# Kernel tuning notes

Measured on AMD Instinct MI355X. Metric: run time of the kernel, lower is better.

The kernel has to match this reference:

```python
import jax, jax.numpy as jnp
import numpy as np

N_WIRES = 9
N_QRAM_LAYERS = 3
N_QCLS_LAYERS = 5

X = jnp.array([[0, 1], [1, 0]], dtype=jnp.complex64)
CNOT = jnp.array([[1, 0, 0, 0], [0, 1, 0, 0], [0, 0, 0, 1], [0, 0, 1, 0]], dtype=jnp.complex64)


def _rx(t):
    c = jnp.cos(t / 2)
    s = jnp.sin(t / 2)
    # works for scalar t -> (2,2) or batched t [B] -> (B,2,2)
    return jnp.stack([jnp.stack([c + 0j, -1j * s], -1), jnp.stack([-1j * s, c + 0j], -1)], -2)


def _ry(t):
    c = jnp.cos(t / 2)
    s = jnp.sin(t / 2)
    return jnp.stack([jnp.stack([c, -s], -1), jnp.stack([s, c], -1)], -2).astype(jnp.complex64)


def _rz(t):
    e = jnp.exp(-0.5j * t)
    f = jnp.exp(0.5j * t)
    z = jnp.zeros_like(e)
    return jnp.stack([jnp.stack([e, z], -1), jnp.stack([z, f], -1)], -2)


def _rot(phi, theta, omega):
    # PennyLane Rot(phi, theta, omega) = RZ(omega) @ RY(theta) @ RZ(phi)
    return _rz(omega) @ _ry(theta) @ _rz(phi)


def _crz(t):
    e = jnp.exp(-0.5j * t)
    f = jnp.exp(0.5j * t)
    one = jnp.ones((), e.dtype)
    return jnp.diag(jnp.stack([one, one, e, f]))


def _crx(t):
    return jnp.eye(4, dtype=jnp.complex64).at[2:, 2:].set(_rx(t))


def apply_1q(state, U, w):
    # state: [B] + (2,)*N_WIRES ; wire w -> axis 1+w
    s = jnp.moveaxis(state, 1 + w, -1)
    if U.ndim == 3:  # per-sample gate (embedding)
        s = jnp.einsum('bij,b...j->b...i', U, s)
    else:
        s = jnp.einsum('ij,...j->...i', U, s)
    return jnp.moveaxis(s, -1, 1 + w)


def apply_2q(state, U, c, t):
    s = jnp.moveaxis(state, (1 + c, 1 + t), (-2, -1))
    shp = s.shape
    s = s.reshape(shp[:-2] + (4,))
    s = jnp.einsum('ij,...j->...i', U, s)
    return jnp.moveaxis(s.reshape(shp), (-2, -1), (1 + c, 1 + t))


def embed(state, adds):
    # AngleEmbedding: RX(adds[:, i]) on wire i
    for i in range(N_WIRES):
        state = apply_1q(state, _rx(adds[:, i]), i)
    return state


def entangle_block(state, p):
    # p: [36] = 4 params per wire-pair step
    j = 0
    for i in range(N_WIRES):
        ip = (i + 1) % N_WIRES
        state = apply_1q(state, _ry(p[j]), i)
        state = apply_1q(state, _ry(p[j + 1]), ip)
        state = apply_2q(state, CNOT, i, ip)
        state = apply_2q(state, _crz(p[j + 2]), i, ip)
        state = apply_1q(state, X, ip)
        state = apply_2q(state, _crx(p[j + 3]), i, ip)
        j += 4
    return state


def sel_layer(state, w, r):
    # one StronglyEntanglingLayers layer: Rot on each wire, then CNOT ring of range r
    for i in range(N_WIRES):
        state = apply_1q(state, _rot(w[i, 0], w[i, 1], w[i, 2]), i)
    for i in range(N_WIRES):
        state = apply_2q(state, CNOT, i, (i + r) % N_WIRES)
    return state


def circuit(adds, params, weights, params2):
    B = adds.shape[0]
    state = jnp.zeros((B,) + (2,) * N_WIRES, jnp.complex64)
    state = state.at[(slice(None),) + (0,) * N_WIRES].set(1.0)
    state = embed(state, adds)
    for l in range(N_QRAM_LAYERS):
        state = entangle_block(state, params[l * 36:(l + 1) * 36])
    for l in range(N_QRAM_LAYERS):
        r = (l % (N_WIRES - 1)) + 1  # PennyLane default ranges
        state = sel_layer(state, weights[l], r)
    for l in range(N_QCLS_LAYERS):
        state = entangle_block(state, params2[l * 36:(l + 1) * 36])
    probs = jnp.abs(state) ** 2
    p = probs.reshape(B, 2, -1).sum(-1)  # marginal over wire 0
    return p[:, 0] - p[:, 1]  # <PauliZ(0)>


def setup_inputs() -> dict:
    key = jax.random.key(0)
    k1, k2, k3, k4 = jax.random.split(key, 4)
    B = 8192
    return {
        'adds': jax.random.normal(k1, (B, N_WIRES), dtype=jnp.float32),
        'params': jax.random.normal(k2, (N_QRAM_LAYERS * 36,), dtype=jnp.float32),
        'weights': jax.random.normal(k3, (N_QRAM_LAYERS, N_WIRES, N_QRAM_LAYERS), dtype=jnp.float32),
        'params2': jax.random.normal(k4, (N_QCLS_LAYERS * 36,), dtype=jnp.float32),
    }


def reference(adds, params, weights, params2):
    return circuit(adds, params, weights, params2)
```

## Files before the change

### kernel.cpp

```cpp
#include <hip/hip_runtime.h>

#define NQ 9
#define NS 512
#define M2 1024

#define COEF_ROT_BASE (72*32)
#define COEF_R3_BASE  (COEF_ROT_BASE + 27*8)
#define COEF_FLOATS   (COEF_R3_BASE + 3*128)

typedef __attribute__((ext_vector_type(8))) short bf16x8;
typedef __attribute__((ext_vector_type(4))) float f32x4;

__device__ inline unsigned short f2bf(float f){
  unsigned int u = __float_as_uint(f);
  u += 0x7fffu + ((u >> 16) & 1u);
  return (unsigned short)(u >> 16);
}


template<int LM>
__device__ inline float lxor(float v){
  if constexpr (LM == 1)
    return __int_as_float(__builtin_amdgcn_mov_dpp(__float_as_int(v), 0xB1, 0xF, 0xF, true));
  else if constexpr (LM == 2)
    return __int_as_float(__builtin_amdgcn_mov_dpp(__float_as_int(v), 0x4E, 0xF, 0xF, true));
  else if constexpr (LM == 3)
    return __int_as_float(__builtin_amdgcn_mov_dpp(__float_as_int(v), 0x1B, 0xF, 0xF, true));
  else if constexpr (LM < 32)
    return __int_as_float(__builtin_amdgcn_ds_swizzle(__float_as_int(v), (LM<<10)|0x1F));
  else
    return __shfl_xor(v, LM);
}

template<int CM, int TM>
__device__ inline void step_h(float& ax, float& ay, int i, float2* buf,
                              const float* g){
  buf[i] = make_float2(ax, ay);
  __syncthreads();
  float2 tv = buf[i ^ TM];
  float2 cv = buf[i ^ CM];
  float2 bv = buf[i ^ (CM ^ TM)];
  int p = ((i & CM) ? 2 : 0) | ((i & TM) ? 1 : 0);
  float4 hx = *(const float4*)(g + p*4);
  float4 hy = *(const float4*)(g + 16 + p*4);
  float ox = ax, oy = ay;
  ax = hx.x*ox - hy.x*oy + hx.y*tv.x - hy.y*tv.y
     + hx.z*cv.x - hy.z*cv.y + hx.w*bv.x - hy.w*bv.y;
  ay = hx.x*oy + hy.x*ox + hx.y*tv.y + hy.y*tv.x
     + hx.z*cv.y + hy.z*cv.x + hx.w*bv.y + hy.w*bv.x;
}

template<int CM, int TM>
__device__ inline void step_swz(float& ax, float& ay, int lane, const float* g){
  float tx = lxor<TM>(ax),      ty = lxor<TM>(ay);
  float cx = lxor<CM>(ax),      cy = lxor<CM>(ay);
  float bx = lxor<(CM^TM)>(ax), by = lxor<(CM^TM)>(ay);
  int p = ((lane & CM) ? 2 : 0) | ((lane & TM) ? 1 : 0);
  float4 hx = *(const float4*)(g + p*4);
  float4 hy = *(const float4*)(g + 16 + p*4);
  float ox = ax, oy = ay;
  ax = hx.x*ox - hy.x*oy + hx.y*tx - hy.y*ty
     + hx.z*cx - hy.z*cy + hx.w*bx - hy.w*by;
  ay = hx.x*oy + hy.x*ox + hx.y*ty + hy.y*tx
     + hx.z*cy + hy.z*cx + hx.w*by + hy.w*bx;
}

__device__ inline void rot3_img(float& ax, float& ay, int i, float2* buf,
                                const float* M){
  buf[i] = make_float2(ax, ay);
  __syncthreads();
  int base = i & 63;
  float nx = 0.f, ny = 0.f;
  #pragma unroll
  for (int q = 0; q < 8; ++q){
    float2 v = buf[(q << 6) | base];
    float mx = M[q*2], my = M[q*2+1];
    nx += mx*v.x - my*v.y;
    ny += mx*v.y + my*v.x;
  }
  ax = nx; ay = ny;
}

template<int LM>
__device__ inline void rot_swz(float& ax, float& ay, int lane, const float* u){
  float px = lxor<LM>(ax), py = lxor<LM>(ay);
  float4 uu = *(const float4*)(u + ((lane & LM) ? 4 : 0));
  float nx = uu.x*ax - uu.y*ay + uu.z*px - uu.w*py;
  float ny = uu.x*ay + uu.y*ax + uu.z*py + uu.w*px;
  ax = nx; ay = ny;
}

__device__ inline void ring_rt(float& ax, float& ay, int i, float2* buf, int R){
  buf[i] = make_float2(ax, ay);
  __syncthreads();
  int s = i;
  for (int k = 8; k >= 0; --k){
    int bc = 8 - k;
    int it = k + R; if (it >= 9) it -= 9;
    int bt = 8 - it;
    s ^= ((s >> bc) & 1) << bt;
  }
  float2 v = buf[s];
  ax = v.x; ay = v.y;
}


template<int I = 0>
__device__ inline void ent_blk(float& ax, float& ay, int i, int lane,
                               float2* bufA, float2* bufB, const float* S){
  const float* g = S + I*32;
  if constexpr      (I == 0) step_h<0x100,0x080>(ax, ay, i, bufA, g);
  else if constexpr (I == 1) step_h<0x080,0x040>(ax, ay, i, bufB, g);
  else if constexpr (I == 2) step_h<0x040,0x020>(ax, ay, i, bufA, g);
  else if constexpr (I == 8) step_h<0x001,0x100>(ax, ay, i, bufB, g);
  else                       step_swz<(1<<(8-I)),(1<<(7-I))>(ax, ay, lane, g);
  if constexpr (I < 8) ent_blk<I+1>(ax, ay, i, lane, bufA, bufB, S);
}

template<int I = 3>
__device__ inline void sel_lane_rots(float& ax, float& ay, int lane,
                                     const float* ub){
  rot_swz<(1<<(8-I))>(ax, ay, lane, ub + I*8);
  if constexpr (I < 8) sel_lane_rots<I+1>(ax, ay, lane, ub);
}

__global__ __launch_bounds__(512) void sim_prep(const float* __restrict__ params,
                                                const float* __restrict__ weights,
                                                const float* __restrict__ params2,
                                                const float* __restrict__ adds,
                                                unsigned short* __restrict__ A2,
                                                unsigned short* __restrict__ cT,
                                                float* __restrict__ out, int B){
  int tid = threadIdx.x;

  if (blockIdx.x >= NS){
    int gid = (blockIdx.x - NS) * 512 + tid;
    int b = gid >> 6;
    int lane = gid & 63;
    if (b < B){
      const float* ab = adds + b * NQ;
      float cw[NQ], sw[NQ];
      #pragma unroll
      for (int w = 0; w < NQ; ++w)
        __sincosf(0.5f * ab[w], &sw[w], &cw[w]);
      float p6 = 1.f;
      #pragma unroll
      for (int w = 0; w < 6; ++w)
        p6 *= ((lane >> (5 - w)) & 1) ? sw[w] : cw[w];
      union { unsigned short u[8]; uint4 v; } pk;
      #pragma unroll
      for (int j = 0; j < 8; ++j){
        float p = p6 * (((j>>2)&1) ? sw[6] : cw[6])
                     * (((j>>1)&1) ? sw[7] : cw[7])
                     * (( j    &1) ? sw[8] : cw[8]);
        pk.u[j] = f2bf(p);
      }
      *(uint4*)(cT + (size_t)b * NS + lane*8) = pk.v;
    }
    if (gid < B) out[gid] = 0.f;
    return;
  }

  __shared__ float2 bufA[512];
  __shared__ float2 bufB[512];
  __shared__ float scoef[COEF_FLOATS];

  if (tid < 72){
    int blk = tid / 9, I = tid % 9;
    const float* p = (blk < 3) ? params + blk*36 : params2 + (blk-3)*36;
    float s0,c0,s1,c1,s2,c2,s3,c3;
    __sincosf(0.5f*p[4*I+0], &s0, &c0);
    __sincosf(0.5f*p[4*I+1], &s1, &c1);
    __sincosf(0.5f*p[4*I+2], &s2, &c2);
    __sincosf(0.5f*p[4*I+3], &s3, &c3);
    float m[4][4] = {
      { c0*c1, -c0*s1, -s0*c1,  s0*s1},
      { c0*s1,  c0*c1, -s0*s1, -s0*c1},
      { s0*c1, -s0*s1,  c0*c1, -c0*s1},
      { s0*s1,  s0*c1,  c0*s1,  c0*c1}};
    float gx[4][4], gy[4][4];
    #pragma unroll
    for (int q = 0; q < 4; ++q){
      gx[0][q] = m[1][q];  gy[0][q] = 0.f;
      gx[1][q] = m[0][q];  gy[1][q] = 0.f;
      gx[2][q] =  c3*c2*m[2][q] - s3*s2*m[3][q];
      gy[2][q] =  c3*s2*m[2][q] - s3*c2*m[3][q];
      gx[3][q] =  s3*s2*m[2][q] + c3*c2*m[3][q];
      gy[3][q] = -(s3*c2*m[2][q] + c3*s2*m[3][q]);
    }
    float* dst = scoef + tid*32;
    #pragma unroll
    for (int pp = 0; pp < 4; ++pp)
      #pragma unroll
      for (int d = 0; d < 4; ++d){
        dst[pp*4+d]    = gx[pp][pp^d];
        dst[16+pp*4+d] = gy[pp][pp^d];
      }
  } else if (tid < 99){
    int r = tid - 72;
    int l = r / 9, i = r % 9;
    const float* w = weights + l*27 + 3*i;
    float phi = w[0], th = w[1], om = w[2];
    float sT,cT,sA,cA,sB,cB;
    __sincosf(0.5f*th, &sT, &cT);
    __sincosf(0.5f*(phi+om), &sA, &cA);
    __sincosf(0.5f*(om-phi), &sB, &cB);
    float* dst = scoef + COEF_ROT_BASE + r*8;
    dst[0] =  cA*cT;  dst[1] = -sA*cT;
    dst[2] = -cB*sT;  dst[3] =  sB*sT;
    dst[4] =  cA*cT;  dst[5] =  sA*cT;
    dst[6] =  cB*sT;  dst[7] =  sB*sT;
  } else if (tid < 123){
    int idx = tid - 99;
    int l = idx >> 3, p = idx & 7;
    float e0x[3], e0y[3], e1x[3], e1y[3];
    #pragma unroll
    for (int w = 0; w < 3; ++w){
      const float* wp = weights + l*27 + 3*w;
      float phi = wp[0], th = wp[1], om = wp[2];
      float sT,cT,sA,cA,sB,cB;
      __sincosf(0.5f*th, &sT, &cT);
      __sincosf(0.5f*(phi+om), &sA, &cA);
      __sincosf(0.5f*(om-phi), &sB, &cB);
      int pw = (p >> (2 - w)) & 1;
      if (pw == 0){ e0x[w] =  cA*cT; e0y[w] = -sA*cT; e1x[w] = -cB*sT; e1y[w] =  sB*sT; }
      else        { e0x[w] =  cB*sT; e0y[w] =  sB*sT; e1x[w] =  cA*cT; e1y[w] =  sA*cT; }
    }
    float* dst = scoef + COEF_R3_BASE + l*128 + p*16;
    #pragma unroll
    for (int q = 0; q < 8; ++q){
      float rx = 1.f, ry = 0.f;
      #pragma unroll
      for (int w = 0; w < 3; ++w){
        int qw = (q >> (2 - w)) & 1;
        float fx = qw ? e1x[w] : e0x[w];
        float fy = qw ? e1y[w] : e0y[w];
        float nx = rx*fx - ry*fy;
        float ny = rx*fy + ry*fx;
        rx = nx; ry = ny;
      }
      dst[q*2]   = rx;
      dst[q*2+1] = ry;
    }
  }
  __syncthreads();

  int t = blockIdx.x;
  int i = tid;
  int lane = tid & 63;
  float ax, ay;
  int pc = __popc((unsigned)t) & 3;
  float prx = (pc==0) ? 1.f : (pc==2 ? -1.f : 0.f);
  float pry = (pc==3) ? 1.f : (pc==1 ? -1.f : 0.f);
  ax = (i == t) ? prx : 0.f;
  ay = (i == t) ? pry : 0.f;

  #pragma unroll 1
  for (int blk = 0; blk < 3; ++blk)
    ent_blk<0>(ax, ay, i, lane, bufA, bufB, scoef + blk*288);
  #pragma unroll 1
  for (int L = 0; L < 3; ++L){
    rot3_img(ax, ay, i, bufA, scoef + COEF_R3_BASE + L*128 + (i>>6)*16);
    sel_lane_rots<3>(ax, ay, lane, scoef + COEF_ROT_BASE + L*72);
    ring_rt(ax, ay, i, bufB, L + 1);
  }
  #pragma unroll 1
  for (int blk = 3; blk < 8; ++blk)
    ent_blk<0>(ax, ay, i, lane, bufA, bufB, scoef + blk*288);

  A2[(size_t)i * NS + t]        = f2bf(ax);
  A2[(size_t)(i + NS) * NS + t] = f2bf(ay);
}

__global__ __launch_bounds__(256) void gemm_out(const unsigned short* __restrict__ A2,
                                                const unsigned short* __restrict__ cT,
                                                float* __restrict__ out){
  int bx = blockIdx.x;
  int by = blockIdx.y;
  int tid = threadIdx.x;
  int wave = tid >> 6, lane = tid & 63;
  int wy = wave >> 1, wx = wave & 1;
  int lane15 = lane & 15, quad = lane >> 4;
  int rowBase = by*128 + wy*64;
  int colBase = bx*128 + wx*64;
  const short* Ap = (const short*)A2;
  const short* Bp = (const short*)cT;

  f32x4 acc[4][4];
  #pragma unroll
  for (int i = 0; i < 4; ++i)
    #pragma unroll
    for (int j = 0; j < 4; ++j)
      acc[i][j] = (f32x4){0.f, 0.f, 0.f, 0.f};

  #pragma unroll 2
  for (int k0 = 0; k0 < NS; k0 += 32){
    bf16x8 a[4], b[4];
    #pragma unroll
    for (int mi = 0; mi < 4; ++mi)
      a[mi] = *(const bf16x8*)(Ap + (size_t)(rowBase + mi*16 + lane15)*NS + k0 + quad*8);
    #pragma unroll
    for (int ni = 0; ni < 4; ++ni)
      b[ni] = *(const bf16x8*)(Bp + (size_t)(colBase + ni*16 + lane15)*NS + k0 + quad*8);
    #pragma unroll
    for (int mi = 0; mi < 4; ++mi)
      #pragma unroll
      for (int ni = 0; ni < 4; ++ni)
        acc[mi][ni] = __builtin_amdgcn_mfma_f32_16x16x32_bf16(a[mi], b[ni], acc[mi][ni], 0, 0, 0);
  }

  float sign = (by & 2) ? -1.f : 1.f;
  #pragma unroll
  for (int ni = 0; ni < 4; ++ni){
    float cs = 0.f;
    #pragma unroll
    for (int mi = 0; mi < 4; ++mi)
      #pragma unroll
      for (int r = 0; r < 4; ++r)
        cs += acc[mi][ni][r] * acc[mi][ni][r];
    cs += __shfl_xor(cs, 16);
    cs += __shfl_xor(cs, 32);
    if (quad == 0)
      atomicAdd(out + colBase + ni*16 + lane15, sign * cs);
  }
}

extern "C" void kernel_launch(void* const* d_in, const int* in_sizes, int n_in,
                              void* d_out, int out_size, void* d_ws, size_t ws_size,
                              hipStream_t stream) {
  const float* adds    = (const float*)d_in[0];
  const float* params  = (const float*)d_in[1];
  const float* weights = (const float*)d_in[2];
  const float* params2 = (const float*)d_in[3];
  float* out = (float*)d_out;
  int B = in_sizes[0] / NQ;

  unsigned short* A2 = (unsigned short*)d_ws;
  unsigned short* cT = A2 + (size_t)M2 * NS;

  int prepBlocks = (B * 64 + 511) / 512;
  hipLaunchKernelGGL(sim_prep, dim3(NS + prepBlocks), dim3(512), 0, stream,
                     params, weights, params2, adds, A2, cT, out, B);
  hipLaunchKernelGGL(gemm_out, dim3(B / 128, 8), dim3(256), 0, stream, A2, cT, out);
}
```

Baseline: 118.2 us.

## Register-block statevector simulation with 4 amplitudes per lane and k-pair A layout

Each simulation block now handles two unitary columns using 128 threads per column, and each lane holds 4 amplitudes in registers. Gates on the middle qubits become register swaps or DPP/swizzle shuffles, so only the top-qubit and cross-wave steps go through LDS with barriers. The CNOT ring is decomposed explicitly instead of using a generic LDS permutation. The A matrix is rewritten in a k-pair-interleaved packed layout so stores coalesce across columns, and the GEMM loads A as 32-bit words with unroll raised to 4. The GEMM's A loads become strided scalar accesses, which risks lowering load efficiency there in exchange for a cheaper simulation kernel.

New measurement: 111.8 us. 1.06x faster.

```diff
diff --git a/kernel.cpp b/kernel.cpp
--- a/kernel.cpp
+++ b/kernel.cpp
@@ -3,6 +3,7 @@
 #define NQ 9
 #define NS 512
 #define M2 1024
+#define NSIMB 256
 
 #define COEF_ROT_BASE (72*32)
 #define COEF_R3_BASE  (COEF_ROT_BASE + 27*8)
@@ -32,99 +33,204 @@
     return __shfl_xor(v, LM);
 }
 
-template<int CM, int TM>
-__device__ inline void step_h(float& ax, float& ay, int i, float2* buf,
-                              const float* g){
-  buf[i] = make_float2(ax, ay);
+template<int M>
+__device__ inline float lx(float v){
+  if constexpr ((M & 63) == 0) return v;
+  else return lxor<(M & 63)>(v);
+}
+
+template<int M>
+__device__ inline void getp(const float (&ox)[4], const float (&oy)[4],
+                            const float2 (&pv)[4], int r, float& qx, float& qy){
+  constexpr int MR = (M >> 6) & 3;
+  float vx, vy;
+  if constexpr ((M & 0x100) != 0){ vx = pv[r^MR].x; vy = pv[r^MR].y; }
+  else                           { vx = ox[r^MR];   vy = oy[r^MR];   }
+  qx = lx<M>(vx); qy = lx<M>(vy);
+}
+
+__device__ inline void xwave(const float (&ax)[4], const float (&ay)[4],
+                             int wvb, int lane, float2* xb, float2 (&pv)[4]){
+  #pragma unroll
+  for (int r = 0; r < 4; ++r) xb[(wvb*4+r)*64 + lane] = make_float2(ax[r], ay[r]);
   __syncthreads();
-  float2 tv = buf[i ^ TM];
-  float2 cv = buf[i ^ CM];
-  float2 bv = buf[i ^ (CM ^ TM)];
-  int p = ((i & CM) ? 2 : 0) | ((i & TM) ? 1 : 0);
-  float4 hx = *(const float4*)(g + p*4);
-  float4 hy = *(const float4*)(g + 16 + p*4);
-  float ox = ax, oy = ay;
-  ax = hx.x*ox - hy.x*oy + hx.y*tv.x - hy.y*tv.y
-     + hx.z*cv.x - hy.z*cv.y + hx.w*bv.x - hy.w*bv.y;
-  ay = hx.x*oy + hy.x*ox + hx.y*tv.y + hy.y*tv.x
-     + hx.z*cv.y + hy.z*cv.x + hx.w*bv.y + hy.w*bv.x;
-}
-
-template<int CM, int TM>
-__device__ inline void step_swz(float& ax, float& ay, int lane, const float* g){
-  float tx = lxor<TM>(ax),      ty = lxor<TM>(ay);
-  float cx = lxor<CM>(ax),      cy = lxor<CM>(ay);
-  float bx = lxor<(CM^TM)>(ax), by = lxor<(CM^TM)>(ay);
-  int p = ((lane & CM) ? 2 : 0) | ((lane & TM) ? 1 : 0);
-  float4 hx = *(const float4*)(g + p*4);
-  float4 hy = *(const float4*)(g + 16 + p*4);
-  float ox = ax, oy = ay;
-  ax = hx.x*ox - hy.x*oy + hx.y*tx - hy.y*ty
-     + hx.z*cx - hy.z*cy + hx.w*bx - hy.w*by;
-  ay = hx.x*oy + hy.x*ox + hx.y*ty + hy.y*tx
-     + hx.z*cy + hy.z*cx + hx.w*by + hy.w*bx;
-}
-
-__device__ inline void rot3_img(float& ax, float& ay, int i, float2* buf,
-                                const float* M){
-  buf[i] = make_float2(ax, ay);
-  __syncthreads();
-  int base = i & 63;
-  float nx = 0.f, ny = 0.f;
-  #pragma unroll
-  for (int q = 0; q < 8; ++q){
-    float2 v = buf[(q << 6) | base];
-    float mx = M[q*2], my = M[q*2+1];
-    nx += mx*v.x - my*v.y;
-    ny += mx*v.y + my*v.x;
-  }
-  ax = nx; ay = ny;
+  #pragma unroll
+  for (int r = 0; r < 4; ++r) pv[r] = xb[((wvb^1)*4+r)*64 + lane];
+}
+
+template<int CM,int TM>
+__device__ inline void stepQ(float (&ax)[4], float (&ay)[4], int wvb, int lane,
+                             float2* xb, const float* g){
+  constexpr bool HX = ((CM | TM) & 0x100) != 0;
+  float2 pv[4];
+  if constexpr (HX) xwave(ax, ay, wvb, lane, xb, pv);
+  float ox[4], oy[4];
+  #pragma unroll
+  for (int r = 0; r < 4; ++r){ ox[r] = ax[r]; oy[r] = ay[r]; }
+  #pragma unroll
+  for (int r = 0; r < 4; ++r){
+    float tx,ty,cx,cy,bx,by;
+    getp<TM>(ox, oy, pv, r, tx, ty);
+    getp<CM>(ox, oy, pv, r, cx, cy);
+    getp<(CM^TM)>(ox, oy, pv, r, bx, by);
+    int i = (wvb << 8) | (r << 6) | lane;
+    int p = ((i & CM) ? 2 : 0) | ((i & TM) ? 1 : 0);
+    float4 hx = *(const float4*)(g + p*4);
+    float4 hy = *(const float4*)(g + 16 + p*4);
+    ax[r] = hx.x*ox[r]-hy.x*oy[r] + hx.y*tx-hy.y*ty + hx.z*cx-hy.z*cy + hx.w*bx-hy.w*by;
+    ay[r] = hx.x*oy[r]+hy.x*ox[r] + hx.y*ty+hy.y*tx + hx.z*cy+hy.z*cx + hx.w*by+hy.w*bx;
+  }
+}
+
+template<int I = 0>
+__device__ inline void ent_blkQ(float (&ax)[4], float (&ay)[4], int wvb, int lane,
+                                float2* ebA, float2* ebB, const float* S){
+  if constexpr      (I == 0) stepQ<0x100,0x080>(ax, ay, wvb, lane, ebA, S);
+  else if constexpr (I == 8) stepQ<0x001,0x100>(ax, ay, wvb, lane, ebB, S + 256);
+  else                       stepQ<(0x100>>I),(0x080>>I)>(ax, ay, wvb, lane, ebA, S + I*32);
+  if constexpr (I < 8) ent_blkQ<I+1>(ax, ay, wvb, lane, ebA, ebB, S);
+}
+
+__device__ inline void rot3Q(float (&ax)[4], float (&ay)[4], int wvb, int lane,
+                             float2* xb, const float* Mt){
+  float2 pv[4];
+  xwave(ax, ay, wvb, lane, xb, pv);
+  bool w1 = (wvb != 0);
+  float l0x[4],l0y[4],l1x[4],l1y[4];
+  #pragma unroll
+  for (int r = 0; r < 4; ++r){
+    l0x[r] = w1 ? pv[r].x : ax[r];  l0y[r] = w1 ? pv[r].y : ay[r];
+    l1x[r] = w1 ? ax[r]   : pv[r].x; l1y[r] = w1 ? ay[r]   : pv[r].y;
+  }
+  #pragma unroll
+  for (int r = 0; r < 4; ++r){
+    const float4* row = (const float4*)(Mt + ((wvb<<2)|r)*16);
+    float4 m0 = row[0], m1 = row[1], m2 = row[2], m3 = row[3];
+    float nx, ny;
+    nx  = m0.x*l0x[0]-m0.y*l0y[0];  ny  = m0.x*l0y[0]+m0.y*l0x[0];
+    nx += m0.z*l0x[1]-m0.w*l0y[1];  ny += m0.z*l0y[1]+m0.w*l0x[1];
+    nx += m1.x*l0x[2]-m1.y*l0y[2];  ny += m1.x*l0y[2]+m1.y*l0x[2];
+    nx += m1.z*l0x[3]-m1.w*l0y[3];  ny += m1.z*l0y[3]+m1.w*l0x[3];
+    nx += m2.x*l1x[0]-m2.y*l1y[0];  ny += m2.x*l1y[0]+m2.y*l1x[0];
+    nx += m2.z*l1x[1]-m2.w*l1y[1];  ny += m2.z*l1y[1]+m2.w*l1x[1];
+    nx += m3.x*l1x[2]-m3.y*l1y[2];  ny += m3.x*l1y[2]+m3.y*l1x[2];
+    nx += m3.z*l1x[3]-m3.w*l1y[3];  ny += m3.z*l1y[3]+m3.w*l1x[3];
+    ax[r] = nx; ay[r] = ny;
+  }
 }
 
 template<int LM>
-__device__ inline void rot_swz(float& ax, float& ay, int lane, const float* u){
-  float px = lxor<LM>(ax), py = lxor<LM>(ay);
+__device__ inline void rotQ(float (&ax)[4], float (&ay)[4], int lane, const float* u){
   float4 uu = *(const float4*)(u + ((lane & LM) ? 4 : 0));
-  float nx = uu.x*ax - uu.y*ay + uu.z*px - uu.w*py;
-  float ny = uu.x*ay + uu.y*ax + uu.z*py + uu.w*px;
-  ax = nx; ay = ny;
-}
-
-__device__ inline void ring_rt(float& ax, float& ay, int i, float2* buf, int R){
-  buf[i] = make_float2(ax, ay);
-  __syncthreads();
-  int s = i;
-  for (int k = 8; k >= 0; --k){
-    int bc = 8 - k;
-    int it = k + R; if (it >= 9) it -= 9;
-    int bt = 8 - it;
-    s ^= ((s >> bc) & 1) << bt;
-  }
-  float2 v = buf[s];
-  ax = v.x; ay = v.y;
-}
-
-
-template<int I = 0>
-__device__ inline void ent_blk(float& ax, float& ay, int i, int lane,
-                               float2* bufA, float2* bufB, const float* S){
-  const float* g = S + I*32;
-  if constexpr      (I == 0) step_h<0x100,0x080>(ax, ay, i, bufA, g);
-  else if constexpr (I == 1) step_h<0x080,0x040>(ax, ay, i, bufB, g);
-  else if constexpr (I == 2) step_h<0x040,0x020>(ax, ay, i, bufA, g);
-  else if constexpr (I == 8) step_h<0x001,0x100>(ax, ay, i, bufB, g);
-  else                       step_swz<(1<<(8-I)),(1<<(7-I))>(ax, ay, lane, g);
-  if constexpr (I < 8) ent_blk<I+1>(ax, ay, i, lane, bufA, bufB, S);
+  #pragma unroll
+  for (int r = 0; r < 4; ++r){
+    float px = lxor<LM>(ax[r]), py = lxor<LM>(ay[r]);
+    float nx = uu.x*ax[r]-uu.y*ay[r] + uu.z*px-uu.w*py;
+    float ny = uu.x*ay[r]+uu.y*ax[r] + uu.z*py+uu.w*px;
+    ax[r] = nx; ay[r] = ny;
+  }
 }
 
 template<int I = 3>
-__device__ inline void sel_lane_rots(float& ax, float& ay, int lane,
-                                     const float* ub){
-  rot_swz<(1<<(8-I))>(ax, ay, lane, ub + I*8);
-  if constexpr (I < 8) sel_lane_rots<I+1>(ax, ay, lane, ub);
-}
-
-__global__ __launch_bounds__(512) void sim_prep(const float* __restrict__ params,
+__device__ inline void sel_rotsQ(float (&ax)[4], float (&ay)[4], int lane, const float* ub){
+  rotQ<(1<<(8-I))>(ax, ay, lane, ub + I*8);
+  if constexpr (I < 8) sel_rotsQ<I+1>(ax, ay, lane, ub);
+}
+
+template<int TR>
+__device__ inline void cn_wr(float (&ax)[4], float (&ay)[4], int wvb){
+  if (wvb){
+    #pragma unroll
+    for (int r = 0; r < 4; ++r) if (!(r & TR)){
+      float t = ax[r]; ax[r] = ax[r|TR]; ax[r|TR] = t;
+      t = ay[r]; ay[r] = ay[r|TR]; ay[r|TR] = t;
+    }
+  }
+}
+template<int TL>
+__device__ inline void cn_wl(float (&ax)[4], float (&ay)[4], int wvb){
+  if (wvb){
+    #pragma unroll
+    for (int r = 0; r < 4; ++r){ ax[r] = lxor<TL>(ax[r]); ay[r] = lxor<TL>(ay[r]); }
+  }
+}
+template<int CR,int TR>
+__device__ inline void cn_rr(float (&ax)[4], float (&ay)[4]){
+  #pragma unroll
+  for (int r = 0; r < 4; ++r) if ((r & CR) && !(r & TR)){
+    float t = ax[r]; ax[r] = ax[r|TR]; ax[r|TR] = t;
+    t = ay[r]; ay[r] = ay[r|TR]; ay[r|TR] = t;
+  }
+}
+template<int CR,int TL>
+__device__ inline void cn_rl(float (&ax)[4], float (&ay)[4]){
+  #pragma unroll
+  for (int r = 0; r < 4; ++r) if (r & CR){ ax[r] = lxor<TL>(ax[r]); ay[r] = lxor<TL>(ay[r]); }
+}
+template<int CL,int TR>
+__device__ inline void cn_lr(float (&ax)[4], float (&ay)[4], int lane){
+  bool c = (lane & CL) != 0;
+  #pragma unroll
+  for (int r = 0; r < 4; ++r) if (!(r & TR)){
+    int rp = r | TR;
+    float t0x = ax[r], t0y = ay[r];
+    ax[r]  = c ? ax[rp] : t0x;  ay[r]  = c ? ay[rp] : t0y;
+    ax[rp] = c ? t0x : ax[rp];  ay[rp] = c ? t0y : ay[rp];
+  }
+}
+template<int CL,int TL>
+__device__ inline void cn_ll(float (&ax)[4], float (&ay)[4], int lane){
+  bool c = (lane & CL) != 0;
+  #pragma unroll
+  for (int r = 0; r < 4; ++r){
+    float px = lxor<TL>(ax[r]), py = lxor<TL>(ay[r]);
+    ax[r] = c ? px : ax[r];  ay[r] = c ? py : ay[r];
+  }
+}
+template<int CL>
+__device__ inline void cn_lw(float (&ax)[4], float (&ay)[4], int wvb, int lane, float2* xb){
+  float2 pv[4];
+  xwave(ax, ay, wvb, lane, xb, pv);
+  bool c = (lane & CL) != 0;
+  #pragma unroll
+  for (int r = 0; r < 4; ++r){ ax[r] = c ? pv[r].x : ax[r]; ay[r] = c ? pv[r].y : ay[r]; }
+}
+
+__device__ inline void ring1(float (&ax)[4], float (&ay)[4], int wvb, int lane, float2* xb){
+  cn_wr<2>(ax,ay,wvb);
+  cn_rr<2,1>(ax,ay);
+  cn_rl<1,32>(ax,ay);
+  cn_ll<32,16>(ax,ay,lane);
+  cn_ll<16,8>(ax,ay,lane);
+  cn_ll<8,4>(ax,ay,lane);
+  cn_ll<4,2>(ax,ay,lane);
+  cn_ll<2,1>(ax,ay,lane);
+  cn_lw<1>(ax,ay,wvb,lane,xb);
+}
+__device__ inline void ring2(float (&ax)[4], float (&ay)[4], int wvb, int lane, float2* xb){
+  cn_wr<1>(ax,ay,wvb);
+  cn_rl<2,32>(ax,ay);
+  cn_rl<1,16>(ax,ay);
+  cn_ll<32,8>(ax,ay,lane);
+  cn_ll<16,4>(ax,ay,lane);
+  cn_ll<8,2>(ax,ay,lane);
+  cn_ll<4,1>(ax,ay,lane);
+  cn_lw<2>(ax,ay,wvb,lane,xb);
+  cn_lr<1,2>(ax,ay,lane);
+}
+__device__ inline void ring3(float (&ax)[4], float (&ay)[4], int wvb, int lane, float2* xb){
+  cn_wl<32>(ax,ay,wvb);
+  cn_rl<2,16>(ax,ay);
+  cn_rl<1,8>(ax,ay);
+  cn_ll<32,4>(ax,ay,lane);
+  cn_ll<16,2>(ax,ay,lane);
+  cn_ll<8,1>(ax,ay,lane);
+  cn_lw<4>(ax,ay,wvb,lane,xb);
+  cn_lr<2,2>(ax,ay,lane);
+  cn_lr<1,1>(ax,ay,lane);
+}
+
+__global__ __launch_bounds__(256) void sim_prep(const float* __restrict__ params,
                                                 const float* __restrict__ weights,
                                                 const float* __restrict__ params2,
                                                 const float* __restrict__ adds,
@@ -133,8 +239,8 @@
                                                 float* __restrict__ out, int B){
   int tid = threadIdx.x;
 
-  if (blockIdx.x >= NS){
-    int gid = (blockIdx.x - NS) * 512 + tid;
+  if (blockIdx.x >= NSIMB){
+    int gid = (blockIdx.x - NSIMB) * 256 + tid;
     int b = gid >> 6;
     int lane = gid & 63;
     if (b < B){
@@ -161,8 +267,8 @@
     return;
   }
 
-  __shared__ float2 bufA[512];
-  __shared__ float2 bufB[512];
+  __shared__ float2 ebufA[1024];
+  __shared__ float2 ebufB[1024];
   __shared__ float scoef[COEF_FLOATS];
 
   if (tid < 72){
@@ -245,31 +351,58 @@
   }
   __syncthreads();
 
-  int t = blockIdx.x;
-  int i = tid;
-  int lane = tid & 63;
-  float ax, ay;
-  int pc = __popc((unsigned)t) & 3;
+  int wid = tid >> 6, lane = tid & 63;
+  int colbit = wid >> 1, wvb = wid & 1;
+  int col = blockIdx.x * 2 + colbit;
+  float2* ebA = ebufA + colbit * 512;
+  float2* ebB = ebufB + colbit * 512;
+
+  float ax[4], ay[4];
+  int pc = __popc((unsigned)col) & 3;
   float prx = (pc==0) ? 1.f : (pc==2 ? -1.f : 0.f);
   float pry = (pc==3) ? 1.f : (pc==1 ? -1.f : 0.f);
-  ax = (i == t) ? prx : 0.f;
-  ay = (i == t) ? pry : 0.f;
+  #pragma unroll
+  for (int r = 0; r < 4; ++r){
+    int i = (wvb<<8) | (r<<6) | lane;
+    ax[r] = (i == col) ? prx : 0.f;
+    ay[r] = (i == col) ? pry : 0.f;
+  }
 
   #pragma unroll 1
   for (int blk = 0; blk < 3; ++blk)
-    ent_blk<0>(ax, ay, i, lane, bufA, bufB, scoef + blk*288);
-  #pragma unroll 1
-  for (int L = 0; L < 3; ++L){
-    rot3_img(ax, ay, i, bufA, scoef + COEF_R3_BASE + L*128 + (i>>6)*16);
-    sel_lane_rots<3>(ax, ay, lane, scoef + COEF_ROT_BASE + L*72);
-    ring_rt(ax, ay, i, bufB, L + 1);
-  }
+    ent_blkQ<0>(ax, ay, wvb, lane, ebA, ebB, scoef + blk*288);
+
+  rot3Q(ax, ay, wvb, lane, ebA, scoef + COEF_R3_BASE + 0*128);
+  sel_rotsQ<3>(ax, ay, lane, scoef + COEF_ROT_BASE + 0*72);
+  ring1(ax, ay, wvb, lane, ebB);
+  rot3Q(ax, ay, wvb, lane, ebA, scoef + COEF_R3_BASE + 1*128);
+  sel_rotsQ<3>(ax, ay, lane, scoef + COEF_ROT_BASE + 1*72);
+  ring2(ax, ay, wvb, lane, ebB);
+  rot3Q(ax, ay, wvb, lane, ebA, scoef + COEF_R3_BASE + 2*128);
+  sel_rotsQ<3>(ax, ay, lane, scoef + COEF_ROT_BASE + 2*72);
+  ring3(ax, ay, wvb, lane, ebB);
+
   #pragma unroll 1
   for (int blk = 3; blk < 8; ++blk)
-    ent_blk<0>(ax, ay, i, lane, bufA, bufB, scoef + blk*288);
-
-  A2[(size_t)i * NS + t]        = f2bf(ax);
-  A2[(size_t)(i + NS) * NS + t] = f2bf(ay);
+    ent_blkQ<0>(ax, ay, wvb, lane, ebA, ebB, scoef + blk*288);
+
+  float2* Lb = ebufA;
+  #pragma unroll
+  for (int r = 0; r < 4; ++r) Lb[(wid*4+r)*64 + lane] = make_float2(ax[r], ay[r]);
+  __syncthreads();
+  int part = wid >> 1;
+  int wb = wid & 1;
+  unsigned int* Aw = (unsigned int*)A2;
+  #pragma unroll
+  for (int r = 0; r < 4; ++r){
+    float2 v0 = Lb[(wb*4+r)*64 + lane];
+    float2 v1 = Lb[((2+wb)*4+r)*64 + lane];
+    float a0 = part ? v0.y : v0.x;
+    float a1 = part ? v1.y : v1.x;
+    unsigned int pk = (unsigned)f2bf(a0) | ((unsigned)f2bf(a1) << 16);
+    int row = (part<<9) + (wb<<8) + (r<<6) + lane;
+    Aw[(size_t)blockIdx.x * 1024 + row] = pk;
+  }
 }
 
 __global__ __launch_bounds__(256) void gemm_out(const unsigned short* __restrict__ A2,
@@ -283,7 +416,7 @@
   int lane15 = lane & 15, quad = lane >> 4;
   int rowBase = by*128 + wy*64;
   int colBase = bx*128 + wx*64;
-  const short* Ap = (const short*)A2;
+  const unsigned int* Aw = (const unsigned int*)A2;
   const short* Bp = (const short*)cT;
 
   f32x4 acc[4][4];
@@ -293,12 +426,18 @@
     for (int j = 0; j < 4; ++j)
       acc[i][j] = (f32x4){0.f, 0.f, 0.f, 0.f};
 
-  #pragma unroll 2
+  #pragma unroll 4
   for (int k0 = 0; k0 < NS; k0 += 32){
-    bf16x8 a[4], b[4];
-    #pragma unroll
-    for (int mi = 0; mi < 4; ++mi)
-      a[mi] = *(const bf16x8*)(Ap + (size_t)(rowBase + mi*16 + lane15)*NS + k0 + quad*8);
+    union { unsigned int w[4]; bf16x8 v; } au[4];
+    bf16x8 b[4];
+    int kb0 = (k0 >> 1) + (quad << 2);
+    #pragma unroll
+    for (int mi = 0; mi < 4; ++mi){
+      int row = rowBase + mi*16 + lane15;
+      #pragma unroll
+      for (int d = 0; d < 4; ++d)
+        au[mi].w[d] = Aw[(size_t)(kb0 + d)*1024 + row];
+    }
     #pragma unroll
     for (int ni = 0; ni < 4; ++ni)
       b[ni] = *(const bf16x8*)(Bp + (size_t)(colBase + ni*16 + lane15)*NS + k0 + quad*8);
@@ -306,7 +445,7 @@
     for (int mi = 0; mi < 4; ++mi)
       #pragma unroll
       for (int ni = 0; ni < 4; ++ni)
-        acc[mi][ni] = __builtin_amdgcn_mfma_f32_16x16x32_bf16(a[mi], b[ni], acc[mi][ni], 0, 0, 0);
+        acc[mi][ni] = __builtin_amdgcn_mfma_f32_16x16x32_bf16(au[mi].v, b[ni], acc[mi][ni], 0, 0, 0);
   }
 
   float sign = (by & 2) ? -1.f : 1.f;
@@ -338,8 +477,8 @@
   unsigned short* A2 = (unsigned short*)d_ws;
   unsigned short* cT = A2 + (size_t)M2 * NS;
 
-  int prepBlocks = (B * 64 + 511) / 512;
-  hipLaunchKernelGGL(sim_prep, dim3(NS + prepBlocks), dim3(512), 0, stream,
+  int prepBlocks = (B * 64 + 255) / 256;
+  hipLaunchKernelGGL(sim_prep, dim3(NSIMB + prepBlocks), dim3(256), 0, stream,
                      params, weights, params2, adds, A2, cT, out, B);
   hipLaunchKernelGGL(gemm_out, dim3(B / 128, 8), dim3(256), 0, stream, A2, cT, out);
 }
```

## Simulate two amplitudes per thread and store the unitary in a k-chunked GEMM layout

Applied to the files above, without the earlier changes.

The simulation kernel now uses 256 threads per column, each holding two state amplitudes. Many gate steps become register swaps or cross-lane ops instead of shared-memory round trips with barriers, and the ring CNOT permutations are decomposed into lane-xor moves. The unitary output is written in a chunked layout of eight k values per row, so GEMM A-loads become contiguous 16-byte reads, and the GEMM loop unroll is raised. This adds register pressure and complex permutation logic that must exactly reproduce the previous ring mapping.

New measurement: 106.1 us. 10.2% less time.

```diff
diff --git a/kernel.cpp b/kernel.cpp
--- a/kernel.cpp
+++ b/kernel.cpp
@@ -3,6 +3,7 @@
 #define NQ 9
 #define NS 512
 #define M2 1024
+#define NSIMB 512
 
 #define COEF_ROT_BASE (72*32)
 #define COEF_R3_BASE  (COEF_ROT_BASE + 27*8)
@@ -32,99 +33,182 @@
     return __shfl_xor(v, LM);
 }
 
-template<int CM, int TM>
-__device__ inline void step_h(float& ax, float& ay, int i, float2* buf,
-                              const float* g){
-  buf[i] = make_float2(ax, ay);
+template<int M>
+__device__ inline float lx(float v){
+  if constexpr ((M & 63) == 0) return v;
+  else return lxor<(M & 63)>(v);
+}
+
+template<int M>
+__device__ inline void getp2(const float (&ox)[2], const float (&oy)[2],
+                             int r, float& qx, float& qy){
+  constexpr int MR = (M >> 6) & 1;
+  qx = lx<M>(ox[r ^ MR]);
+  qy = lx<M>(oy[r ^ MR]);
+}
+
+template<int CM,int TM>
+__device__ inline void stepQ2(float (&ax)[2], float (&ay)[2], int w, int lane,
+                              float2* xb, const float* g){
+  constexpr bool HX = ((CM | TM) & 0x180) != 0;
+  float ox[2] = {ax[0], ax[1]}, oy[2] = {ay[0], ay[1]};
+  float tx[2],ty[2],cx[2],cy[2],bx[2],by[2];
+  if constexpr (HX){
+    #pragma unroll
+    for (int r = 0; r < 2; ++r) xb[(w<<7)|(r<<6)|lane] = make_float2(ox[r], oy[r]);
+    __syncthreads();
+    #pragma unroll
+    for (int r = 0; r < 2; ++r){
+      int i = (w<<7)|(r<<6)|lane;
+      float2 tv = xb[i^TM], cv = xb[i^CM], bv = xb[i^(CM^TM)];
+      tx[r]=tv.x; ty[r]=tv.y; cx[r]=cv.x; cy[r]=cv.y; bx[r]=bv.x; by[r]=bv.y;
+    }
+  } else {
+    #pragma unroll
+    for (int r = 0; r < 2; ++r){
+      getp2<TM>(ox, oy, r, tx[r], ty[r]);
+      getp2<CM>(ox, oy, r, cx[r], cy[r]);
+      getp2<(CM^TM)>(ox, oy, r, bx[r], by[r]);
+    }
+  }
+  #pragma unroll
+  for (int r = 0; r < 2; ++r){
+    int i = (w<<7)|(r<<6)|lane;
+    int p = ((i & CM) ? 2 : 0) | ((i & TM) ? 1 : 0);
+    float4 hx = *(const float4*)(g + p*4);
+    float4 hy = *(const float4*)(g + 16 + p*4);
+    ax[r] = hx.x*ox[r]-hy.x*oy[r] + hx.y*tx[r]-hy.y*ty[r]
+          + hx.z*cx[r]-hy.z*cy[r] + hx.w*bx[r]-hy.w*by[r];
+    ay[r] = hx.x*oy[r]+hy.x*ox[r] + hx.y*ty[r]+hy.y*tx[r]
+          + hx.z*cy[r]+hy.z*cx[r] + hx.w*by[r]+hy.w*bx[r];
+  }
+}
+
+__device__ inline void ent_blk2(float (&ax)[2], float (&ay)[2], int w, int lane,
+                                float2* bX, float2* bY, const float* S){
+  stepQ2<0x100,0x080>(ax, ay, w, lane, bX, S);
+  stepQ2<0x080,0x040>(ax, ay, w, lane, bY, S + 32);
+  stepQ2<0x040,0x020>(ax, ay, w, lane, bX, S + 64);
+  stepQ2<0x020,0x010>(ax, ay, w, lane, bX, S + 96);
+  stepQ2<0x010,0x008>(ax, ay, w, lane, bX, S + 128);
+  stepQ2<0x008,0x004>(ax, ay, w, lane, bX, S + 160);
+  stepQ2<0x004,0x002>(ax, ay, w, lane, bX, S + 192);
+  stepQ2<0x002,0x001>(ax, ay, w, lane, bX, S + 224);
+  stepQ2<0x001,0x100>(ax, ay, w, lane, bX, S + 256);
+}
+
+__device__ inline void rot3Q2(float (&ax)[2], float (&ay)[2], int w, int lane,
+                              float2* xb, const float* Mt){
+  #pragma unroll
+  for (int r = 0; r < 2; ++r) xb[(w<<7)|(r<<6)|lane] = make_float2(ax[r], ay[r]);
   __syncthreads();
-  float2 tv = buf[i ^ TM];
-  float2 cv = buf[i ^ CM];
-  float2 bv = buf[i ^ (CM ^ TM)];
-  int p = ((i & CM) ? 2 : 0) | ((i & TM) ? 1 : 0);
-  float4 hx = *(const float4*)(g + p*4);
-  float4 hy = *(const float4*)(g + 16 + p*4);
-  float ox = ax, oy = ay;
-  ax = hx.x*ox - hy.x*oy + hx.y*tv.x - hy.y*tv.y
-     + hx.z*cv.x - hy.z*cv.y + hx.w*bv.x - hy.w*bv.y;
-  ay = hx.x*oy + hy.x*ox + hx.y*tv.y + hy.y*tv.x
-     + hx.z*cv.y + hy.z*cv.x + hx.w*bv.y + hy.w*bv.x;
-}
-
-template<int CM, int TM>
-__device__ inline void step_swz(float& ax, float& ay, int lane, const float* g){
-  float tx = lxor<TM>(ax),      ty = lxor<TM>(ay);
-  float cx = lxor<CM>(ax),      cy = lxor<CM>(ay);
-  float bx = lxor<(CM^TM)>(ax), by = lxor<(CM^TM)>(ay);
-  int p = ((lane & CM) ? 2 : 0) | ((lane & TM) ? 1 : 0);
-  float4 hx = *(const float4*)(g + p*4);
-  float4 hy = *(const float4*)(g + 16 + p*4);
-  float ox = ax, oy = ay;
-  ax = hx.x*ox - hy.x*oy + hx.y*tx - hy.y*ty
-     + hx.z*cx - hy.z*cy + hx.w*bx - hy.w*by;
-  ay = hx.x*oy + hy.x*ox + hx.y*ty + hy.y*tx
-     + hx.z*cy + hy.z*cx + hx.w*by + hy.w*bx;
-}
-
-__device__ inline void rot3_img(float& ax, float& ay, int i, float2* buf,
-                                const float* M){
-  buf[i] = make_float2(ax, ay);
+  #pragma unroll
+  for (int r = 0; r < 2; ++r){
+    const float* M = Mt + ((w<<1)|r)*16;
+    float nx = 0.f, ny = 0.f;
+    #pragma unroll
+    for (int q = 0; q < 8; ++q){
+      float2 v = xb[(q<<6)|lane];
+      float mx = M[q*2], my = M[q*2+1];
+      nx += mx*v.x - my*v.y;
+      ny += mx*v.y + my*v.x;
+    }
+    ax[r] = nx; ay[r] = ny;
+  }
+}
+
+template<int LM>
+__device__ inline void rotQ2(float (&ax)[2], float (&ay)[2], int lane, const float* u){
+  float4 uu = *(const float4*)(u + ((lane & LM) ? 4 : 0));
+  #pragma unroll
+  for (int r = 0; r < 2; ++r){
+    float px = lxor<LM>(ax[r]), py = lxor<LM>(ay[r]);
+    float nx = uu.x*ax[r]-uu.y*ay[r] + uu.z*px-uu.w*py;
+    float ny = uu.x*ay[r]+uu.y*ax[r] + uu.z*py+uu.w*px;
+    ax[r] = nx; ay[r] = ny;
+  }
+}
+
+template<int I = 3>
+__device__ inline void sel_rots2(float (&ax)[2], float (&ay)[2], int lane, const float* ub){
+  rotQ2<(1<<(8-I))>(ax, ay, lane, ub + I*8);
+  if constexpr (I < 8) sel_rots2<I+1>(ax, ay, lane, ub);
+}
+
+__device__ inline void swap2(float& a, float& b){ float t=a; a=b; b=t; }
+
+template<int CL,int TL>
+__device__ inline void cn_ll2(float (&ax)[2], float (&ay)[2], int lane){
+  bool c = (lane & CL) != 0;
+  #pragma unroll
+  for (int r = 0; r < 2; ++r){
+    float px = lxor<TL>(ax[r]), py = lxor<TL>(ay[r]);
+    ax[r] = c ? px : ax[r];  ay[r] = c ? py : ay[r];
+  }
+}
+
+template<int C1,int T1,int C2,int T2>
+__device__ inline void cn_perm(float (&ax)[2], float (&ay)[2], int w, int lane, float2* xb){
+  #pragma unroll
+  for (int r = 0; r < 2; ++r) xb[(w<<7)|(r<<6)|lane] = make_float2(ax[r], ay[r]);
   __syncthreads();
-  int base = i & 63;
-  float nx = 0.f, ny = 0.f;
-  #pragma unroll
-  for (int q = 0; q < 8; ++q){
-    float2 v = buf[(q << 6) | base];
-    float mx = M[q*2], my = M[q*2+1];
-    nx += mx*v.x - my*v.y;
-    ny += mx*v.y + my*v.x;
-  }
-  ax = nx; ay = ny;
-}
-
-template<int LM>
-__device__ inline void rot_swz(float& ax, float& ay, int lane, const float* u){
-  float px = lxor<LM>(ax), py = lxor<LM>(ay);
-  float4 uu = *(const float4*)(u + ((lane & LM) ? 4 : 0));
-  float nx = uu.x*ax - uu.y*ay + uu.z*px - uu.w*py;
-  float ny = uu.x*ay + uu.y*ax + uu.z*py + uu.w*px;
-  ax = nx; ay = ny;
-}
-
-__device__ inline void ring_rt(float& ax, float& ay, int i, float2* buf, int R){
-  buf[i] = make_float2(ax, ay);
-  __syncthreads();
-  int s = i;
-  for (int k = 8; k >= 0; --k){
-    int bc = 8 - k;
-    int it = k + R; if (it >= 9) it -= 9;
-    int bt = 8 - it;
-    s ^= ((s >> bc) & 1) << bt;
-  }
-  float2 v = buf[s];
-  ax = v.x; ay = v.y;
-}
-
-
-template<int I = 0>
-__device__ inline void ent_blk(float& ax, float& ay, int i, int lane,
-                               float2* bufA, float2* bufB, const float* S){
-  const float* g = S + I*32;
-  if constexpr      (I == 0) step_h<0x100,0x080>(ax, ay, i, bufA, g);
-  else if constexpr (I == 1) step_h<0x080,0x040>(ax, ay, i, bufB, g);
-  else if constexpr (I == 2) step_h<0x040,0x020>(ax, ay, i, bufA, g);
-  else if constexpr (I == 8) step_h<0x001,0x100>(ax, ay, i, bufB, g);
-  else                       step_swz<(1<<(8-I)),(1<<(7-I))>(ax, ay, lane, g);
-  if constexpr (I < 8) ent_blk<I+1>(ax, ay, i, lane, bufA, bufB, S);
-}
-
-template<int I = 3>
-__device__ inline void sel_lane_rots(float& ax, float& ay, int lane,
-                                     const float* ub){
-  rot_swz<(1<<(8-I))>(ax, ay, lane, ub + I*8);
-  if constexpr (I < 8) sel_lane_rots<I+1>(ax, ay, lane, ub);
-}
-
-__global__ __launch_bounds__(512) void sim_prep(const float* __restrict__ params,
+  #pragma unroll
+  for (int r = 0; r < 2; ++r){
+    int i = (w<<7)|(r<<6)|lane;
+    int j = i ^ (((i>>C1)&1)<<T1);
+    if constexpr (C2 >= 0) j ^= ((i>>C2)&1)<<T2;
+    float2 v = xb[j];
+    ax[r] = v.x; ay[r] = v.y;
+  }
+}
+
+__device__ inline void ring1_2(float (&ax)[2], float (&ay)[2], int w, int lane,
+                               float2* xA, float2* xB){
+  cn_perm<8,7,-1,0>(ax, ay, w, lane, xA);
+  if (w & 1){ swap2(ax[0],ax[1]); swap2(ay[0],ay[1]); }
+  ax[1]=lxor<32>(ax[1]); ay[1]=lxor<32>(ay[1]);
+  cn_ll2<32,16>(ax,ay,lane);
+  cn_ll2<16,8>(ax,ay,lane);
+  cn_ll2<8,4>(ax,ay,lane);
+  cn_ll2<4,2>(ax,ay,lane);
+  cn_ll2<2,1>(ax,ay,lane);
+  cn_perm<0,8,-1,0>(ax, ay, w, lane, xB);
+}
+__device__ inline void ring2_2(float (&ax)[2], float (&ay)[2], int w, int lane, float2* xB){
+  if (w & 2){ swap2(ax[0],ax[1]); swap2(ay[0],ay[1]); }
+  if (w & 1){
+    #pragma unroll
+    for (int r=0;r<2;++r){ ax[r]=lxor<32>(ax[r]); ay[r]=lxor<32>(ay[r]); }
+  }
+  ax[1]=lxor<16>(ax[1]); ay[1]=lxor<16>(ay[1]);
+  cn_ll2<32,8>(ax,ay,lane);
+  cn_ll2<16,4>(ax,ay,lane);
+  cn_ll2<8,2>(ax,ay,lane);
+  cn_ll2<4,1>(ax,ay,lane);
+  cn_perm<1,8,0,7>(ax, ay, w, lane, xB);
+}
+__device__ inline void ring3_2(float (&ax)[2], float (&ay)[2], int w, int lane, float2* xB){
+  if (w & 2){
+    #pragma unroll
+    for (int r=0;r<2;++r){ ax[r]=lxor<32>(ax[r]); ay[r]=lxor<32>(ay[r]); }
+  }
+  if (w & 1){
+    #pragma unroll
+    for (int r=0;r<2;++r){ ax[r]=lxor<16>(ax[r]); ay[r]=lxor<16>(ay[r]); }
+  }
+  ax[1]=lxor<8>(ax[1]); ay[1]=lxor<8>(ay[1]);
+  cn_ll2<32,4>(ax,ay,lane);
+  cn_ll2<16,2>(ax,ay,lane);
+  cn_ll2<8,1>(ax,ay,lane);
+  cn_perm<2,8,1,7>(ax, ay, w, lane, xB);
+  bool c = (lane & 1) != 0;
+  float t0x = ax[0], t0y = ay[0];
+  ax[0] = c ? ax[1] : ax[0];  ay[0] = c ? ay[1] : ay[0];
+  ax[1] = c ? t0x   : ax[1];  ay[1] = c ? t0y   : ay[1];
+}
+
+
+__global__ __launch_bounds__(256) void sim_prep(const float* __restrict__ params,
                                                 const float* __restrict__ weights,
                                                 const float* __restrict__ params2,
                                                 const float* __restrict__ adds,
@@ -133,8 +217,8 @@
                                                 float* __restrict__ out, int B){
   int tid = threadIdx.x;
 
-  if (blockIdx.x >= NS){
-    int gid = (blockIdx.x - NS) * 512 + tid;
+  if (blockIdx.x >= NSIMB){
+    int gid = (blockIdx.x - NSIMB) * 256 + tid;
     int b = gid >> 6;
     int lane = gid & 63;
     if (b < B){
@@ -161,8 +245,8 @@
     return;
   }
 
-  __shared__ float2 bufA[512];
-  __shared__ float2 bufB[512];
+  __shared__ float2 ebufA[512];
+  __shared__ float2 ebufB[512];
   __shared__ float scoef[COEF_FLOATS];
 
   if (tid < 72){
@@ -245,31 +329,50 @@
   }
   __syncthreads();
 
-  int t = blockIdx.x;
-  int i = tid;
-  int lane = tid & 63;
-  float ax, ay;
-  int pc = __popc((unsigned)t) & 3;
+  int w = tid >> 6, lane = tid & 63;
+  int col = blockIdx.x;
+
+  float ax[2], ay[2];
+  int pc = __popc((unsigned)col) & 3;
   float prx = (pc==0) ? 1.f : (pc==2 ? -1.f : 0.f);
   float pry = (pc==3) ? 1.f : (pc==1 ? -1.f : 0.f);
-  ax = (i == t) ? prx : 0.f;
-  ay = (i == t) ? pry : 0.f;
-
-  #pragma unroll 1
-  for (int blk = 0; blk < 3; ++blk)
-    ent_blk<0>(ax, ay, i, lane, bufA, bufB, scoef + blk*288);
-  #pragma unroll 1
-  for (int L = 0; L < 3; ++L){
-    rot3_img(ax, ay, i, bufA, scoef + COEF_R3_BASE + L*128 + (i>>6)*16);
-    sel_lane_rots<3>(ax, ay, lane, scoef + COEF_ROT_BASE + L*72);
-    ring_rt(ax, ay, i, bufB, L + 1);
-  }
-  #pragma unroll 1
-  for (int blk = 3; blk < 8; ++blk)
-    ent_blk<0>(ax, ay, i, lane, bufA, bufB, scoef + blk*288);
-
-  A2[(size_t)i * NS + t]        = f2bf(ax);
-  A2[(size_t)(i + NS) * NS + t] = f2bf(ay);
+  #pragma unroll
+  for (int r = 0; r < 2; ++r){
+    int i = (w<<7) | (r<<6) | lane;
+    ax[r] = (i == col) ? prx : 0.f;
+    ay[r] = (i == col) ? pry : 0.f;
+  }
+
+  ent_blk2(ax, ay, w, lane, ebufA, ebufB, scoef + 0*288);
+  ent_blk2(ax, ay, w, lane, ebufB, ebufA, scoef + 1*288);
+  ent_blk2(ax, ay, w, lane, ebufA, ebufB, scoef + 2*288);
+
+  rot3Q2(ax, ay, w, lane, ebufB, scoef + COEF_R3_BASE + 0*128);
+  sel_rots2<3>(ax, ay, lane, scoef + COEF_ROT_BASE + 0*72);
+  ring1_2(ax, ay, w, lane, ebufA, ebufB);
+
+  rot3Q2(ax, ay, w, lane, ebufA, scoef + COEF_R3_BASE + 1*128);
+  sel_rots2<3>(ax, ay, lane, scoef + COEF_ROT_BASE + 1*72);
+  ring2_2(ax, ay, w, lane, ebufB);
+
+  rot3Q2(ax, ay, w, lane, ebufA, scoef + COEF_R3_BASE + 2*128);
+  sel_rots2<3>(ax, ay, lane, scoef + COEF_ROT_BASE + 2*72);
+  ring3_2(ax, ay, w, lane, ebufB);
+
+  ent_blk2(ax, ay, w, lane, ebufA, ebufB, scoef + 3*288);
+  ent_blk2(ax, ay, w, lane, ebufB, ebufA, scoef + 4*288);
+  ent_blk2(ax, ay, w, lane, ebufA, ebufB, scoef + 5*288);
+  ent_blk2(ax, ay, w, lane, ebufB, ebufA, scoef + 6*288);
+  ent_blk2(ax, ay, w, lane, ebufA, ebufB, scoef + 7*288);
+
+  int c = col >> 3, sub = col & 7;
+  size_t base = (size_t)c * 1024;
+  #pragma unroll
+  for (int r = 0; r < 2; ++r){
+    int i = (w<<7) | (r<<6) | lane;
+    A2[(base + i)*8 + sub]       = f2bf(ax[r]);
+    A2[(base + 512 + i)*8 + sub] = f2bf(ay[r]);
+  }
 }
 
 __global__ __launch_bounds__(256) void gemm_out(const unsigned short* __restrict__ A2,
@@ -283,7 +386,7 @@
   int lane15 = lane & 15, quad = lane >> 4;
   int rowBase = by*128 + wy*64;
   int colBase = bx*128 + wx*64;
-  const short* Ap = (const short*)A2;
+  const bf16x8* Ap8 = (const bf16x8*)A2;
   const short* Bp = (const short*)cT;
 
   f32x4 acc[4][4];
@@ -293,12 +396,13 @@
     for (int j = 0; j < 4; ++j)
       acc[i][j] = (f32x4){0.f, 0.f, 0.f, 0.f};
 
-  #pragma unroll 2
+  #pragma unroll 4
   for (int k0 = 0; k0 < NS; k0 += 32){
     bf16x8 a[4], b[4];
+    int c = (k0 >> 3) + quad;
     #pragma unroll
     for (int mi = 0; mi < 4; ++mi)
-      a[mi] = *(const bf16x8*)(Ap + (size_t)(rowBase + mi*16 + lane15)*NS + k0 + quad*8);
+      a[mi] = Ap8[(size_t)c*1024 + rowBase + mi*16 + lane15];
     #pragma unroll
     for (int ni = 0; ni < 4; ++ni)
       b[ni] = *(const bf16x8*)(Bp + (size_t)(colBase + ni*16 + lane15)*NS + k0 + quad*8);
@@ -338,8 +442,8 @@
   unsigned short* A2 = (unsigned short*)d_ws;
   unsigned short* cT = A2 + (size_t)M2 * NS;
 
-  int prepBlocks = (B * 64 + 511) / 512;
-  hipLaunchKernelGGL(sim_prep, dim3(NS + prepBlocks), dim3(512), 0, stream,
+  int prepBlocks = (B * 64 + 255) / 256;
+  hipLaunchKernelGGL(sim_prep, dim3(NSIMB + prepBlocks), dim3(256), 0, stream,
                      params, weights, params2, adds, A2, cT, out, B);
   hipLaunchKernelGGL(gemm_out, dim3(B / 128, 8), dim3(256), 0, stream, A2, cT, out);
 }
```
